# Kernel optimization log

Hardware: AMD Instinct MI355X
Metric: run time of the kernel (lower is better)

The kernel has to match this reference:

```python
import jax, jax.numpy as jnp
import numpy as np


def setup_inputs() -> dict:
    key = jax.random.key(0)
    k1, k2 = jax.random.split(key)
    B, C, H, W = 8, 64, 128, 128
    C_w, ks = 8, 3
    x = jax.random.normal(k1, (B, C, H, W), dtype=jnp.float32)
    w = jax.random.normal(k2, (B, C_w, ks * ks, H, W), dtype=jnp.float32)
    return {"x": x, "w": w}


def _ska_2d(x, w):
    # x: (B,C,H,W); w: (B,C_w,ks^2,H,W); groups = C // C_w
    B, C, H, W = x.shape
    C_w, ks2 = w.shape[1], w.shape[2]
    ks = int(round(np.sqrt(ks2)))
    pad = ks // 2
    groups = C // C_w
    x_pad = jnp.pad(x, ((0, 0), (0, 0), (pad, pad), (pad, pad)))
    # Gather shifted views instead of materializing a giant unfold copy; order
    # matches F.unfold (kernel row-major: i outer, j inner).
    patches = jnp.stack(
        [x_pad[:, :, i:i + H, j:j + W] for i in range(ks) for j in range(ks)],
        axis=2,
    )  # (B, C, ks^2, H, W)
    # Split channels as (groups, C_w): output channel c = g*C_w + cw uses weight channel cw.
    p = patches.reshape(B, groups, C_w, ks2, H, W)
    out = jnp.einsum('bgckhw,bckhw->bgchw', p, w)  # sum over kernel positions k
    return out.reshape(B, C, H, W)


def reference(x, w):
    return _ska_2d(x, w)
```

## Files before the change

kernel.cpp:

```cpp
#include <hip/hip_runtime.h>


#define SKA_H 128
#define SKA_W 128
#define SKA_HW (SKA_H * SKA_W)

__global__ __launch_bounds__(256) void SKA_44830868635847_kernel(
        const float* __restrict__ x,
        const float* __restrict__ wgt,
        float* __restrict__ out) {
    int tid = blockIdx.x * 256 + threadIdx.x;
    int w4 = tid & 31;
    int h  = (tid >> 5) & 127;
    int cw = (tid >> 12) & 7;
    int b  = tid >> 15;
    int w0 = w4 * 4;

    const float* wbase = wgt + ((size_t)(b * 8 + cw) * 9) * SKA_HW + h * SKA_W + w0;
    float4 wv[9];
#pragma unroll
    for (int k = 0; k < 9; ++k)
        wv[k] = *(const float4*)(wbase + (size_t)k * SKA_HW);

    const bool has_left  = (w0 != 0);
    const bool has_right = (w0 != SKA_W - 4);

#pragma unroll
    for (int g = 0; g < 8; ++g) {
        int c = g * 8 + cw;
        const float* xc = x + (size_t)(b * 64 + c) * SKA_HW;
        float4 acc = make_float4(0.f, 0.f, 0.f, 0.f);
#pragma unroll
        for (int i = 0; i < 3; ++i) {
            int hr = h + i - 1;
            if (hr < 0 || hr >= SKA_H) continue;
            const float* xr = xc + hr * SKA_W + w0;
            float4 mid = *(const float4*)xr;
            float xl = has_left  ? xr[-1] : 0.f;
            float xr4 = has_right ? xr[4]  : 0.f;
            float4 wl = wv[i * 3 + 0];
            float4 wm = wv[i * 3 + 1];
            float4 wr = wv[i * 3 + 2];
            acc.x += wl.x * xl;
            acc.y += wl.y * mid.x;
            acc.z += wl.z * mid.y;
            acc.w += wl.w * mid.z;
            acc.x += wm.x * mid.x;
            acc.y += wm.y * mid.y;
            acc.z += wm.z * mid.z;
            acc.w += wm.w * mid.w;
            acc.x += wr.x * mid.y;
            acc.y += wr.y * mid.z;
            acc.z += wr.z * mid.w;
            acc.w += wr.w * xr4;
        }
        *(float4*)(out + (size_t)(b * 64 + c) * SKA_HW + h * SKA_W + w0) = acc;
    }
}

extern "C" void kernel_launch(void* const* d_in, const int* in_sizes, int n_in,
                              void* d_out, int out_size, void* d_ws, size_t ws_size,
                              hipStream_t stream) {
    const float* x   = (const float*)d_in[0];
    const float* wgt = (const float*)d_in[1];
    float* out = (float*)d_out;

    const int total = 8 * 8 * 128 * 32;
    SKA_44830868635847_kernel<<<total / 256, 256, 0, stream>>>(x, wgt, out);
}
```

Measured before the change: 114.3 us.

## Stage x row tiles with halo in LDS and use wave shuffles for neighbors

Each block now covers 8 output rows of one (b, cw) across all 8 groups. It first loads the 10-row haloed input slab for those 8 channels into shared memory, so each input row is fetched from global memory once per tile instead of up to three times from overlapping row reads. Left and right neighbor pixels now come from wavefront shuffles instead of extra scalar global loads, and the launch bounds request 4 blocks per CU. The cost is 40 KB of LDS per block and a barrier, which may limit occupancy, and the total global traffic is already dominated by the weight and output streams.

```diff
diff --git a/kernel.cpp b/kernel.cpp
--- a/kernel.cpp
+++ b/kernel.cpp
@@ -1,60 +1,71 @@
 #include <hip/hip_runtime.h>
 
 
-#define SKA_H 128
 #define SKA_W 128
-#define SKA_HW (SKA_H * SKA_W)
+#define SKA_HW (128 * 128)
+#define TILE_ROWS 8
+#define STAGE_ROWS 10
 
-__global__ __launch_bounds__(256) void SKA_44830868635847_kernel(
+__global__ __launch_bounds__(256, 4) void SKA_44830868635847_kernel(
         const float* __restrict__ x,
         const float* __restrict__ wgt,
         float* __restrict__ out) {
-    int tid = blockIdx.x * 256 + threadIdx.x;
-    int w4 = tid & 31;
-    int h  = (tid >> 5) & 127;
-    int cw = (tid >> 12) & 7;
-    int b  = tid >> 15;
-    int w0 = w4 * 4;
+    __shared__ float lds[8 * STAGE_ROWS * SKA_W];
 
+    const int t     = threadIdx.x;
+    const int bid   = blockIdx.x;
+    const int htile = bid & 15;
+    const int cw    = (bid >> 4) & 7;
+    const int b     = bid >> 7;
+    const int h0    = htile * TILE_ROWS;
+
+    const int w4 = t & 31;
+    const int hl = t >> 5;
+    const int h  = h0 + hl;
+    const int w0 = w4 * 4;
     const float* wbase = wgt + ((size_t)(b * 8 + cw) * 9) * SKA_HW + h * SKA_W + w0;
     float4 wv[9];
 #pragma unroll
     for (int k = 0; k < 9; ++k)
         wv[k] = *(const float4*)(wbase + (size_t)k * SKA_HW);
 
-    const bool has_left  = (w0 != 0);
-    const bool has_right = (w0 != SKA_W - 4);
+    const float* xb = x + (size_t)(b * 64 + cw) * SKA_HW;
+#pragma unroll
+    for (int rep = 0; rep < 10; ++rep) {
+        int idx = rep * 256 + t;
+        int ch  = idx / 320;
+        int rem = idx - ch * 320;
+        int r   = rem >> 5;
+        int c4  = rem & 31;
+        int xrow = h0 - 1 + r;
+        float4 v = make_float4(0.f, 0.f, 0.f, 0.f);
+        if ((unsigned)xrow < 128u)
+            v = *(const float4*)(xb + (size_t)ch * 8 * SKA_HW + xrow * SKA_W + c4 * 4);
+        *(float4*)&lds[(ch * STAGE_ROWS + r) * SKA_W + c4 * 4] = v;
+    }
+    __syncthreads();
 
+    const size_t obase = (size_t)(b * 64 + cw) * SKA_HW + (size_t)h * SKA_W + w0;
 #pragma unroll
     for (int g = 0; g < 8; ++g) {
-        int c = g * 8 + cw;
-        const float* xc = x + (size_t)(b * 64 + c) * SKA_HW;
         float4 acc = make_float4(0.f, 0.f, 0.f, 0.f);
 #pragma unroll
         for (int i = 0; i < 3; ++i) {
-            int hr = h + i - 1;
-            if (hr < 0 || hr >= SKA_H) continue;
-            const float* xr = xc + hr * SKA_W + w0;
-            float4 mid = *(const float4*)xr;
-            float xl = has_left  ? xr[-1] : 0.f;
-            float xr4 = has_right ? xr[4]  : 0.f;
+            const float* lrow = &lds[(g * STAGE_ROWS + hl + i) * SKA_W + w0];
+            float4 mid = *(const float4*)lrow;
+            float xl  = __shfl_up(mid.w, 1);
+            xl  = (w4 == 0)  ? 0.f : xl;
+            float xr4 = __shfl_down(mid.x, 1);
+            xr4 = (w4 == 31) ? 0.f : xr4;
             float4 wl = wv[i * 3 + 0];
             float4 wm = wv[i * 3 + 1];
             float4 wr = wv[i * 3 + 2];
-            acc.x += wl.x * xl;
-            acc.y += wl.y * mid.x;
-            acc.z += wl.z * mid.y;
-            acc.w += wl.w * mid.z;
-            acc.x += wm.x * mid.x;
-            acc.y += wm.y * mid.y;
-            acc.z += wm.z * mid.z;
-            acc.w += wm.w * mid.w;
-            acc.x += wr.x * mid.y;
-            acc.y += wr.y * mid.z;
-            acc.z += wr.z * mid.w;
-            acc.w += wr.w * xr4;
+            acc.x += wl.x * xl    + wm.x * mid.x + wr.x * mid.y;
+            acc.y += wl.y * mid.x + wm.y * mid.y + wr.y * mid.z;
+            acc.z += wl.z * mid.y + wm.z * mid.z + wr.z * mid.w;
+            acc.w += wl.w * mid.z + wm.w * mid.w + wr.w * xr4;
         }
-        *(float4*)(out + (size_t)(b * 64 + c) * SKA_HW + h * SKA_W + w0) = acc;
+        *(float4*)(out + obase + (size_t)g * 8 * SKA_HW) = acc;
     }
 }
 
@@ -65,6 +76,5 @@
     const float* wgt = (const float*)d_in[1];
     float* out = (float*)d_out;
 
-    const int total = 8 * 8 * 128 * 32;
-    SKA_44830868635847_kernel<<<total / 256, 256, 0, stream>>>(x, wgt, out);
+    SKA_44830868635847_kernel<<<1024, 256, 0, stream>>>(x, wgt, out);
 }
```

New measurement: 106.9 us. -6.5%, faster.
